# Kernel tuning notes

Measured on AMD Instinct MI355X. Metric: run time of the kernel, lower is better.

Reference implementation:

```python
import jax, jax.numpy as jnp
import numpy as np

NUM_ROUTING = 3
EPS = 1e-9

def squash(s):
    # s: [..., V]; v = s * ||s||^2 / (1+||s||^2) / ||s||
    sq = jnp.sum(s * s, axis=-1, keepdims=True)
    return s * sq / (1.0 + sq) / jnp.sqrt(sq + EPS)

def setup_inputs() -> dict:
    key = jax.random.key(0)
    k1, k2 = jax.random.split(key)
    B, I, U = 128, 2048, 16   # batch, input capsules, input units
    J, V = 32, 16             # output capsules, output units
    x = jax.random.normal(k1, (B, I, U), dtype=jnp.float32)
    W = jax.random.normal(k2, (I, J, V, U), dtype=jnp.float32) * 0.05
    bias = jnp.zeros((J, V), dtype=jnp.float32)
    return {"x": x, "W": W, "bias": bias}

def reference(x, W, bias):
    # Capsule transform: votes u_hat[b,i,j,v] = sum_u x[b,i,u] * W[i,j,v,u]
    u = jnp.einsum('biu,ijvu->bijv', x, W)  # [B, I, J, V]
    b = jnp.zeros(u.shape[:3], dtype=u.dtype)  # routing logits [B, I, J]
    v = None
    for r in range(NUM_ROUTING):
        c = jax.nn.softmax(b, axis=2)                      # coupling over output caps
        s = jnp.einsum('bij,bijv->bjv', c, u) + bias       # [B, J, V]
        v = squash(s)
        if r < NUM_ROUTING - 1:
            b = b + jnp.einsum('bijv,bjv->bij', u, v)      # agreement update
    return v  # activation='linear' -> identity
```

## Files before the change

kernel.cpp:

```cpp
#include <hip/hip_runtime.h>
#include <math.h>

#define NB 128
#define NI 2048
#define NU 16
#define NJ 32
#define NV 16
#define NJV 512

#define BI 16
#define IC (NI / BI)

typedef __attribute__((ext_vector_type(8))) short  short8v;
typedef __attribute__((ext_vector_type(4))) float  float4v;

#define GLD16(gp, lp) __builtin_amdgcn_global_load_lds( \
    (const __attribute__((address_space(1))) unsigned int*)(gp), \
    (__attribute__((address_space(3))) unsigned int*)(lp), 16, 0, 0)

__device__ __forceinline__ unsigned int bf16rne(float f) {
    unsigned int u = __float_as_uint(f);
    return (u + 0x7FFFu + ((u >> 16) & 1u)) >> 16;
}
__device__ __forceinline__ unsigned int bfp(float a, float b) {
    return bf16rne(a) | (bf16rne(b) << 16);
}

__global__ __launch_bounds__(256)
void convert_W_kernel(const float* __restrict__ W, uint4* __restrict__ Wb) {
    int T = blockIdx.x * 256 + threadIdx.x;
    int h = T & 31, t = (T >> 5) & 31, i = T >> 10;
    int c = h & 15, g1 = h >> 4;
    const float* src = W + ((size_t)(i * 512 + t * 16 + c) * 16 + g1 * 8);
    float4 f0 = *(const float4*)src;
    float4 f1 = *(const float4*)(src + 4);
    uint4 o;
    o.x = bfp(f0.x, f0.y); o.y = bfp(f0.z, f0.w);
    o.z = bfp(f1.x, f1.y); o.w = bfp(f1.z, f1.w);
    Wb[T] = o;
}

__global__ __launch_bounds__(256)
void convert_x_kernel(const float* __restrict__ x, uint4* __restrict__ xb) {
    int T = blockIdx.x * 256 + threadIdx.x;
    int h = T & 31, i = (T >> 5) & 2047, bt = T >> 16;
    int c = h & 15, g1 = h >> 4;
    const float* src = x + ((size_t)(bt * 16 + c) * 2048 + i) * 16 + g1 * 8;
    float4 f0 = *(const float4*)src;
    float4 f1 = *(const float4*)(src + 4);
    uint4 o;
    o.x = bfp(f0.x, f0.y); o.y = bfp(f0.z, f0.w);
    o.z = bfp(f1.x, f1.y); o.w = bfp(f1.z, f1.w);
    xb[T] = o;
}

template<int MODE>
__global__ __launch_bounds__(256, 1)
void pass_mfma(const char* __restrict__ Wb, const char* __restrict__ xb,
               const float* __restrict__ Vacc, float* __restrict__ part)
{
    __shared__ float smem[8320];
    const int tid  = threadIdx.x;
    const int lane = tid & 63;
    const int wave = tid >> 6;
    const int c = lane & 15, g = lane >> 4;
    const int jh = wave & 1;
    const int bt = blockIdx.y * 2 + (wave >> 1);
    const int ibase = blockIdx.x * BI;
    const int hh = (g & 1) * 16 + c;

    const char* Bbase = xb + (size_t)bt * 1048576 + (size_t)ibase * 512 + hh * 16;

#define STAGE(i_, buf_)                                                         \
    {                                                                           \
        const char* srcp = Wb + (size_t)(i_) * 16384 + tid * 16;                \
        _Pragma("unroll")                                                       \
        for (int p = 0; p < 4; ++p)                                             \
            GLD16(srcp + p * 4096, &smem[(buf_) * 4096 + p * 1024 + tid * 4]);  \
    }

    STAGE(ibase, 0);
    float4v vc[16];
    if (MODE) {
        const float* vbase = Vacc + ((size_t)(bt * 16 + c) * 512 + jh * 256 + g * 4);
#pragma unroll
        for (int t = 0; t < 16; ++t)
            vc[t] = *reinterpret_cast<const float4v*>(vbase + t * 16);
    }
    short8v bcur = *reinterpret_cast<const short8v*>(Bbase);

    float4v s_loc[16];
#pragma unroll
    for (int t = 0; t < 16; ++t) s_loc[t] = (float4v)(0.f);

    for (int il = 0; il < BI; ++il) {
        const int cur = il & 1;

        if (il < BI - 1) {
            STAGE(ibase + il + 1, cur ^ 1);
            asm volatile("s_waitcnt vmcnt(4)" ::: "memory");
        } else {
            asm volatile("s_waitcnt vmcnt(0)" ::: "memory");
        }
        __builtin_amdgcn_s_barrier();
        asm volatile("" ::: "memory");

        short8v bnxt = bcur;
        if (il < BI - 1)
            bnxt = *reinterpret_cast<const short8v*>(Bbase + (size_t)(il + 1) * 512);

        if (MODE == 0) {
#pragma unroll
            for (int t = 0; t < 16; ++t) {
                short8v a = *reinterpret_cast<const short8v*>(
                    &smem[cur * 4096 + jh * 2048 + t * 128 + hh * 4]);
                s_loc[t] = __builtin_amdgcn_mfma_f32_16x16x32_bf16(a, bcur, s_loc[t], 0, 0, 0);
            }
            asm volatile("s_waitcnt lgkmcnt(0)" ::: "memory");
            __builtin_amdgcn_s_barrier();
            asm volatile("" ::: "memory");
        } else {
            float4v uv[16];
#pragma unroll
            for (int t = 0; t < 16; ++t) {
                short8v a = *reinterpret_cast<const short8v*>(
                    &smem[cur * 4096 + jh * 2048 + t * 128 + hh * 4]);
                uv[t] = __builtin_amdgcn_mfma_f32_16x16x32_bf16(a, bcur, (float4v)(0.f), 0, 0, 0);
            }

            float p[16];
#pragma unroll
            for (int t = 0; t < 16; ++t) {
                float a = uv[t][0] * vc[t][0];
                a = fmaf(uv[t][1], vc[t][1], a);
                a = fmaf(uv[t][2], vc[t][2], a);
                a = fmaf(uv[t][3], vc[t][3], a);
                p[t] = a;
            }
#pragma unroll
            for (int t = 0; t < 16; ++t)
                p[t] += __int_as_float(__builtin_amdgcn_ds_swizzle(__float_as_int(p[t]), 0x401F));
#pragma unroll
            for (int t = 0; t < 16; ++t)
                p[t] += __shfl_xor(p[t], 32, 64);

#pragma unroll
            for (int t = 0; t < 16; ++t) p[t] = __expf(p[t] * 0.5f);
            float s01 = ((p[0] + p[1]) + (p[2] + p[3])) + ((p[4] + p[5]) + (p[6] + p[7]));
            float s23 = ((p[8] + p[9]) + (p[10] + p[11])) + ((p[12] + p[13]) + (p[14] + p[15]));
            float sl = s01 + s23;

            const int par = il & 1;
            if (lane < 16) smem[8192 + par * 64 + wave * 16 + lane] = sl;
            asm volatile("s_waitcnt lgkmcnt(0)" ::: "memory");
            __builtin_amdgcn_s_barrier();
            asm volatile("" ::: "memory");
            float so = smem[8192 + par * 64 + (wave ^ 1) * 16 + c];
            float inv = __builtin_amdgcn_rcpf(sl + so) * 0.5f;

#pragma unroll
            for (int t = 0; t < 16; ++t) {
                float cc = p[t] * inv;
#pragma unroll
                for (int r = 0; r < 4; ++r)
                    s_loc[t][r] = fmaf(cc, uv[t][r], s_loc[t][r]);
            }
        }
        bcur = bnxt;
    }

    const float scale = (MODE == 0) ? (1.0f / 64.0f) : 1.0f;
    float* pb = part + ((size_t)(blockIdx.y * IC + blockIdx.x)) * 16384;
#pragma unroll
    for (int t = 0; t < 16; ++t) {
        float4v o = s_loc[t] * scale;
        *reinterpret_cast<float4v*>(&pb[((wave * 16 + t) * 64 + lane) * 4]) = o;
    }
#undef STAGE
}

__global__ __launch_bounds__(64)
void reduce_squash(const float* __restrict__ part, const float* __restrict__ bias,
                   float* __restrict__ Vacc, float* __restrict__ out, int mode)
{
    const int tid = threadIdx.x;
    const int sfq = blockIdx.x * 64 + tid;
    const int by = sfq >> 12, sf = sfq & 4095;
    const int wave = sf >> 10, t = (sf >> 6) & 15;
    const int c = tid & 15, g = (tid >> 4) & 3;

    const float* src = part + (size_t)by * (IC * 16384) + (size_t)sf * 4;
    float4v a0 = (float4v)(0.f), a1 = (float4v)(0.f), a2 = (float4v)(0.f), a3 = (float4v)(0.f);
    for (int ic = 0; ic < IC; ic += 4) {
        a0 += *reinterpret_cast<const float4v*>(src + (size_t)(ic + 0) * 16384);
        a1 += *reinterpret_cast<const float4v*>(src + (size_t)(ic + 1) * 16384);
        a2 += *reinterpret_cast<const float4v*>(src + (size_t)(ic + 2) * 16384);
        a3 += *reinterpret_cast<const float4v*>(src + (size_t)(ic + 3) * 16384);
    }
    float4v s = (a0 + a1) + (a2 + a3);

    const int b = by * 32 + (wave >> 1) * 16 + c;
    const int j = (wave & 1) * 16 + t;
    const float4v bi = *reinterpret_cast<const float4v*>(bias + j * 16 + g * 4);
    s += bi;

    float sq = s[0]*s[0] + s[1]*s[1] + s[2]*s[2] + s[3]*s[3];
    sq += __int_as_float(__builtin_amdgcn_ds_swizzle(__float_as_int(sq), 0x401F));
    sq += __shfl_xor(sq, 32, 64);

    float m = sq / (1.0f + sq) * __builtin_amdgcn_rsqf(sq + 1e-9f);
    float4v val = s * m;

    float* dst = (mode == 2) ? out : Vacc;
    float4v* dp = reinterpret_cast<float4v*>(dst + (size_t)b * 512 + j * 16 + g * 4);
    if (mode == 1) {
        float4v old = *reinterpret_cast<const float4v*>(
            Vacc + (size_t)b * 512 + j * 16 + g * 4);
        *dp = old + val;
    } else {
        *dp = val;
    }
}

__global__ __launch_bounds__(256)
void squash_kernel(const float* __restrict__ s_in, const float* __restrict__ bias,
                   float* __restrict__ Vacc, float* __restrict__ out, int mode)
{
    int idx = blockIdx.x * 256 + threadIdx.x;
    float s = s_in[idx] + bias[idx & (NJV - 1)];
    float sq = s * s;
#pragma unroll
    for (int m = 1; m < 16; m <<= 1) sq += __shfl_xor(sq, m, 64);
    float val = s * sq / (1.0f + sq) / sqrtf(sq + 1e-9f);
    if (mode == 0)      Vacc[idx] = val;
    else if (mode == 1) Vacc[idx] += val;
    else                out[idx]  = val;
}

#define FBI 16
#define FIC (NI / FBI)

template<int CTRL>
__device__ __forceinline__ float dpp_add(float x) {
    int t = __builtin_amdgcn_update_dpp(0, __float_as_int(x), CTRL, 0xf, 0xf, true);
    return x + __int_as_float(t);
}
__device__ __forceinline__ float red16(float x) {
    x = dpp_add<0xB1>(x); x = dpp_add<0x4E>(x);
    x = dpp_add<0x141>(x); x = dpp_add<0x140>(x);
    return x;
}

template<int MODE>
__global__ __launch_bounds__(256, 1)
void pass_fb(const float* __restrict__ x, const float* __restrict__ W,
             const float* __restrict__ Vacc, float* __restrict__ s_out)
{
    __shared__ float Wlds[2][8192];
    const int tid = threadIdx.x, lane = tid & 63, wave = tid >> 6;
    const int ibase = blockIdx.x * FBI;
    const int b0 = blockIdx.y * 32 + wave * 8;
    const int soff = ((tid >> 4) & 3) * 1024 + (tid & 15) * 64 + (tid >> 6) * 16;
    const char* Wbp = (const char*)W;
#define FSTAGE(i_, buf_) { const char* srcp = Wbp + (size_t)(i_) * 32768 + soff; \
    _Pragma("unroll") for (int p = 0; p < 8; ++p) \
        GLD16(srcp + p * 4096, &Wlds[buf_][p * 1024 + tid * 4]); }
    float vacc[8][8];
    if (MODE) {
#pragma unroll
        for (int b = 0; b < 8; ++b)
#pragma unroll
            for (int k = 0; k < 8; ++k)
                vacc[b][k] = Vacc[(size_t)(b0 + b) * NJV + lane + 64 * k];
    }
    float s_local[8][8];
#pragma unroll
    for (int b = 0; b < 8; ++b)
#pragma unroll
        for (int k = 0; k < 8; ++k) s_local[b][k] = 0.f;
    float uv[8][8];
    FSTAGE(ibase, 0);
    for (int il = 0; il < FBI; ++il) {
        const int i = ibase + il, cur = il & 1;
        if (il < FBI - 1) {
            FSTAGE(i + 1, cur ^ 1);
            asm volatile("s_waitcnt vmcnt(8)" ::: "memory");
        } else {
            asm volatile("s_waitcnt vmcnt(0)" ::: "memory");
        }
        __builtin_amdgcn_s_barrier();
        asm volatile("" ::: "memory");
#pragma unroll
        for (int q = 0; q < 4; ++q) {
            float4 xv[8];
#pragma unroll
            for (int b = 0; b < 8; ++b)
                xv[b] = *(const float4*)(x + ((size_t)(b0 + b) * NI + i) * NU + q * 4);
#pragma unroll
            for (int k = 0; k < 8; ++k) {
                float4 w = *(const float4*)&Wlds[cur][(k * 4 + q) * 256 + lane * 4];
#pragma unroll
                for (int b = 0; b < 8; ++b) {
                    if (MODE) {
                        float a = (q == 0) ? xv[b].x * w.x : fmaf(xv[b].x, w.x, uv[b][k]);
                        a = fmaf(xv[b].y, w.y, a); a = fmaf(xv[b].z, w.z, a);
                        a = fmaf(xv[b].w, w.w, a); uv[b][k] = a;
                    } else {
                        float a = fmaf(xv[b].x, w.x, s_local[b][k]);
                        a = fmaf(xv[b].y, w.y, a); a = fmaf(xv[b].z, w.z, a);
                        a = fmaf(xv[b].w, w.w, a); s_local[b][k] = a;
                    }
                }
            }
        }
        if (MODE) {
#pragma unroll
            for (int b = 0; b < 8; ++b) {
                float p8[8];
#pragma unroll
                for (int k = 0; k < 8; ++k) p8[k] = uv[b][k] * vacc[b][k];
#pragma unroll
                for (int k = 0; k < 8; ++k) p8[k] = red16(p8[k]);
                float sl = 0.f;
#pragma unroll
                for (int k = 0; k < 8; ++k) { p8[k] = __expf(p8[k]); sl += p8[k]; }
                sl += __int_as_float(__builtin_amdgcn_ds_swizzle(__float_as_int(sl), 0x401F));
                sl += __int_as_float(__builtin_amdgcn_ds_bpermute((lane ^ 32) << 2,
                                                                  __float_as_int(sl)));
                float inv = __builtin_amdgcn_rcpf(sl);
#pragma unroll
                for (int k = 0; k < 8; ++k)
                    s_local[b][k] = fmaf(p8[k] * inv, uv[b][k], s_local[b][k]);
            }
        }
        asm volatile("" ::: "memory");
        __builtin_amdgcn_s_barrier();
        asm volatile("" ::: "memory");
    }
    const float scale = (MODE == 0) ? (1.0f / NJ) : 1.0f;
#pragma unroll
    for (int b = 0; b < 8; ++b)
#pragma unroll
        for (int k = 0; k < 8; ++k)
            atomicAdd(&s_out[(size_t)(b0 + b) * NJV + lane + 64 * k],
                      s_local[b][k] * scale);
#undef FSTAGE
}

extern "C" void kernel_launch(void* const* d_in, const int* in_sizes, int n_in,
                              void* d_out, int out_size, void* d_ws, size_t ws_size,
                              hipStream_t stream)
{
    const float* x    = (const float*)d_in[0];
    const float* W    = (const float*)d_in[1];
    const float* bias = (const float*)d_in[2];
    float* out = (float*)d_out;

    float* s_buf = (float*)d_ws;
    float* Vacc  = s_buf + NB * NJV;
    char*  Wb16  = (char*)(Vacc + NB * NJV);
    char*  xb16  = Wb16 + (size_t)33554432;
    float* part  = (float*)(xb16 + (size_t)8388608);

    const size_t NEED = 2u * NB * NJV * 4 + 33554432u + 8388608u + 33554432u;

    dim3 sgrid(NB * NJV / 256), sblk(256);
    size_t s_bytes = (size_t)NB * NJV * sizeof(float);

    if (ws_size >= NEED) {
        convert_W_kernel<<<8192, 256, 0, stream>>>(W, (uint4*)Wb16);
        convert_x_kernel<<<2048, 256, 0, stream>>>(x, (uint4*)xb16);

        dim3 grid(IC, 4), blk(256);
        dim3 rgrid(256), rblk(64);

        pass_mfma<0><<<grid, blk, 0, stream>>>(Wb16, xb16, Vacc, part);
        reduce_squash<<<rgrid, rblk, 0, stream>>>(part, bias, Vacc, out, 0);

        pass_mfma<1><<<grid, blk, 0, stream>>>(Wb16, xb16, Vacc, part);
        reduce_squash<<<rgrid, rblk, 0, stream>>>(part, bias, Vacc, out, 1);

        pass_mfma<1><<<grid, blk, 0, stream>>>(Wb16, xb16, Vacc, part);
        reduce_squash<<<rgrid, rblk, 0, stream>>>(part, bias, Vacc, out, 2);
    } else {
        dim3 grid(FIC, 4), blk(256);

        (void)hipMemsetAsync(s_buf, 0, s_bytes, stream);
        pass_fb<0><<<grid, blk, 0, stream>>>(x, W, Vacc, s_buf);
        squash_kernel<<<sgrid, sblk, 0, stream>>>(s_buf, bias, Vacc, out, 0);

        (void)hipMemsetAsync(s_buf, 0, s_bytes, stream);
        pass_fb<1><<<grid, blk, 0, stream>>>(x, W, Vacc, s_buf);
        squash_kernel<<<sgrid, sblk, 0, stream>>>(s_buf, bias, Vacc, out, 1);

        (void)hipMemsetAsync(s_buf, 0, s_bytes, stream);
        pass_fb<1><<<grid, blk, 0, stream>>>(x, W, Vacc, s_buf);
        squash_kernel<<<sgrid, sblk, 0, stream>>>(s_buf, bias, Vacc, out, 2);
    }
}
```

Measured before the change: 281.8 us.

## Split MFMA pass work across 4 j-quarters per block and parallelize reduction

Each block of the routing pass now handles a single 16-batch tile, with its four waves each covering a quarter of the output capsules, instead of two batch tiles times two j-halves. The grid doubles in y and the launch bounds allow two blocks per CU, cutting per-thread register arrays in half to raise occupancy. The softmax denominator is now combined from four per-wave partial sums in LDS. The reduce kernel uses four waves per block that each sum a quarter of the partial slices and combine them through LDS, giving more parallel loads. In exchange, each W tile staged in LDS is reused by fewer batch tiles, so W is read from L2 twice as often.

```diff
diff --git a/kernel.cpp b/kernel.cpp
--- a/kernel.cpp
+++ b/kernel.cpp
@@ -55,17 +55,16 @@
 }
 
 template<int MODE>
-__global__ __launch_bounds__(256, 1)
+__global__ __launch_bounds__(256, 2)
 void pass_mfma(const char* __restrict__ Wb, const char* __restrict__ xb,
                const float* __restrict__ Vacc, float* __restrict__ part)
 {
     __shared__ float smem[8320];
     const int tid  = threadIdx.x;
     const int lane = tid & 63;
-    const int wave = tid >> 6;
+    const int jq   = tid >> 6;
     const int c = lane & 15, g = lane >> 4;
-    const int jh = wave & 1;
-    const int bt = blockIdx.y * 2 + (wave >> 1);
+    const int bt = blockIdx.y;
     const int ibase = blockIdx.x * BI;
     const int hh = (g & 1) * 16 + c;
 
@@ -80,18 +79,18 @@
     }
 
     STAGE(ibase, 0);
-    float4v vc[16];
+    float4v vc[8];
     if (MODE) {
-        const float* vbase = Vacc + ((size_t)(bt * 16 + c) * 512 + jh * 256 + g * 4);
-#pragma unroll
-        for (int t = 0; t < 16; ++t)
+        const float* vbase = Vacc + ((size_t)(bt * 16 + c) * 512 + jq * 128 + g * 4);
+#pragma unroll
+        for (int t = 0; t < 8; ++t)
             vc[t] = *reinterpret_cast<const float4v*>(vbase + t * 16);
     }
     short8v bcur = *reinterpret_cast<const short8v*>(Bbase);
 
-    float4v s_loc[16];
-#pragma unroll
-    for (int t = 0; t < 16; ++t) s_loc[t] = (float4v)(0.f);
+    float4v s_loc[8];
+#pragma unroll
+    for (int t = 0; t < 8; ++t) s_loc[t] = (float4v)(0.f);
 
     for (int il = 0; il < BI; ++il) {
         const int cur = il & 1;
@@ -111,26 +110,26 @@
 
         if (MODE == 0) {
 #pragma unroll
-            for (int t = 0; t < 16; ++t) {
+            for (int t = 0; t < 8; ++t) {
                 short8v a = *reinterpret_cast<const short8v*>(
-                    &smem[cur * 4096 + jh * 2048 + t * 128 + hh * 4]);
+                    &smem[cur * 4096 + (jq * 8 + t) * 128 + hh * 4]);
                 s_loc[t] = __builtin_amdgcn_mfma_f32_16x16x32_bf16(a, bcur, s_loc[t], 0, 0, 0);
             }
             asm volatile("s_waitcnt lgkmcnt(0)" ::: "memory");
             __builtin_amdgcn_s_barrier();
             asm volatile("" ::: "memory");
         } else {
-            float4v uv[16];
-#pragma unroll
-            for (int t = 0; t < 16; ++t) {
+            float4v uv[8];
+#pragma unroll
+            for (int t = 0; t < 8; ++t) {
                 short8v a = *reinterpret_cast<const short8v*>(
-                    &smem[cur * 4096 + jh * 2048 + t * 128 + hh * 4]);
+                    &smem[cur * 4096 + (jq * 8 + t) * 128 + hh * 4]);
                 uv[t] = __builtin_amdgcn_mfma_f32_16x16x32_bf16(a, bcur, (float4v)(0.f), 0, 0, 0);
             }
 
-            float p[16];
-#pragma unroll
-            for (int t = 0; t < 16; ++t) {
+            float p[8];
+#pragma unroll
+            for (int t = 0; t < 8; ++t) {
                 float a = uv[t][0] * vc[t][0];
                 a = fmaf(uv[t][1], vc[t][1], a);
                 a = fmaf(uv[t][2], vc[t][2], a);
@@ -138,28 +137,29 @@
                 p[t] = a;
             }
 #pragma unroll
-            for (int t = 0; t < 16; ++t)
+            for (int t = 0; t < 8; ++t)
                 p[t] += __int_as_float(__builtin_amdgcn_ds_swizzle(__float_as_int(p[t]), 0x401F));
 #pragma unroll
-            for (int t = 0; t < 16; ++t)
+            for (int t = 0; t < 8; ++t)
                 p[t] += __shfl_xor(p[t], 32, 64);
 
 #pragma unroll
-            for (int t = 0; t < 16; ++t) p[t] = __expf(p[t] * 0.5f);
-            float s01 = ((p[0] + p[1]) + (p[2] + p[3])) + ((p[4] + p[5]) + (p[6] + p[7]));
-            float s23 = ((p[8] + p[9]) + (p[10] + p[11])) + ((p[12] + p[13]) + (p[14] + p[15]));
-            float sl = s01 + s23;
+            for (int t = 0; t < 8; ++t) p[t] = __expf(p[t] * 0.5f);
+            float sl = ((p[0] + p[1]) + (p[2] + p[3])) + ((p[4] + p[5]) + (p[6] + p[7]));
 
             const int par = il & 1;
-            if (lane < 16) smem[8192 + par * 64 + wave * 16 + lane] = sl;
+            if (lane < 16) smem[8192 + par * 64 + jq * 16 + lane] = sl;
             asm volatile("s_waitcnt lgkmcnt(0)" ::: "memory");
             __builtin_amdgcn_s_barrier();
             asm volatile("" ::: "memory");
-            float so = smem[8192 + par * 64 + (wave ^ 1) * 16 + c];
-            float inv = __builtin_amdgcn_rcpf(sl + so) * 0.5f;
-
-#pragma unroll
-            for (int t = 0; t < 16; ++t) {
+            float q0 = smem[8192 + par * 64 + 0 * 16 + c];
+            float q1 = smem[8192 + par * 64 + 1 * 16 + c];
+            float q2 = smem[8192 + par * 64 + 2 * 16 + c];
+            float q3 = smem[8192 + par * 64 + 3 * 16 + c];
+            float inv = __builtin_amdgcn_rcpf((q0 + q1) + (q2 + q3)) * 0.5f;
+
+#pragma unroll
+            for (int t = 0; t < 8; ++t) {
                 float cc = p[t] * inv;
 #pragma unroll
                 for (int r = 0; r < 4; ++r)
@@ -170,55 +170,71 @@
     }
 
     const float scale = (MODE == 0) ? (1.0f / 64.0f) : 1.0f;
-    float* pb = part + ((size_t)(blockIdx.y * IC + blockIdx.x)) * 16384;
-#pragma unroll
-    for (int t = 0; t < 16; ++t) {
+    float* pb = part + ((size_t)(blockIdx.y * IC + blockIdx.x)) * 8192;
+#pragma unroll
+    for (int t = 0; t < 8; ++t) {
         float4v o = s_loc[t] * scale;
-        *reinterpret_cast<float4v*>(&pb[((wave * 16 + t) * 64 + lane) * 4]) = o;
+        *reinterpret_cast<float4v*>(&pb[((jq * 8 + t) * 64 + lane) * 4]) = o;
     }
 #undef STAGE
 }
 
-__global__ __launch_bounds__(64)
+__global__ __launch_bounds__(256)
 void reduce_squash(const float* __restrict__ part, const float* __restrict__ bias,
                    float* __restrict__ Vacc, float* __restrict__ out, int mode)
 {
+    __shared__ float lds[3][64][4];
     const int tid = threadIdx.x;
-    const int sfq = blockIdx.x * 64 + tid;
-    const int by = sfq >> 12, sf = sfq & 4095;
-    const int wave = sf >> 10, t = (sf >> 6) & 15;
-    const int c = tid & 15, g = (tid >> 4) & 3;
-
-    const float* src = part + (size_t)by * (IC * 16384) + (size_t)sf * 4;
-    float4v a0 = (float4v)(0.f), a1 = (float4v)(0.f), a2 = (float4v)(0.f), a3 = (float4v)(0.f);
-    for (int ic = 0; ic < IC; ic += 4) {
-        a0 += *reinterpret_cast<const float4v*>(src + (size_t)(ic + 0) * 16384);
-        a1 += *reinterpret_cast<const float4v*>(src + (size_t)(ic + 1) * 16384);
-        a2 += *reinterpret_cast<const float4v*>(src + (size_t)(ic + 2) * 16384);
-        a3 += *reinterpret_cast<const float4v*>(src + (size_t)(ic + 3) * 16384);
+    const int w = tid >> 6, l = tid & 63;
+    const int sfq = blockIdx.x * 64 + l;
+    const int bt = sfq >> 11, sf = sfq & 2047;
+    const int j = sf >> 6;
+    const int c = l & 15, g = (l >> 4) & 3;
+
+    const float* src = part + (size_t)bt * (IC * 8192) + (size_t)sf * 4
+                            + (size_t)(w * 32) * 8192;
+    float4v a0 = (float4v)(0.f), a1 = (float4v)(0.f),
+            a2 = (float4v)(0.f), a3 = (float4v)(0.f);
+#pragma unroll
+    for (int ic = 0; ic < 32; ic += 4) {
+        a0 += *reinterpret_cast<const float4v*>(src + (size_t)(ic + 0) * 8192);
+        a1 += *reinterpret_cast<const float4v*>(src + (size_t)(ic + 1) * 8192);
+        a2 += *reinterpret_cast<const float4v*>(src + (size_t)(ic + 2) * 8192);
+        a3 += *reinterpret_cast<const float4v*>(src + (size_t)(ic + 3) * 8192);
     }
     float4v s = (a0 + a1) + (a2 + a3);
 
-    const int b = by * 32 + (wave >> 1) * 16 + c;
-    const int j = (wave & 1) * 16 + t;
-    const float4v bi = *reinterpret_cast<const float4v*>(bias + j * 16 + g * 4);
-    s += bi;
-
-    float sq = s[0]*s[0] + s[1]*s[1] + s[2]*s[2] + s[3]*s[3];
-    sq += __int_as_float(__builtin_amdgcn_ds_swizzle(__float_as_int(sq), 0x401F));
-    sq += __shfl_xor(sq, 32, 64);
-
-    float m = sq / (1.0f + sq) * __builtin_amdgcn_rsqf(sq + 1e-9f);
-    float4v val = s * m;
-
-    float* dst = (mode == 2) ? out : Vacc;
-    float4v* dp = reinterpret_cast<float4v*>(dst + (size_t)b * 512 + j * 16 + g * 4);
-    if (mode == 1) {
-        float4v old = *reinterpret_cast<const float4v*>(
-            Vacc + (size_t)b * 512 + j * 16 + g * 4);
-        *dp = old + val;
-    } else {
-        *dp = val;
+    if (w != 0) {
+        lds[w - 1][l][0] = s[0]; lds[w - 1][l][1] = s[1];
+        lds[w - 1][l][2] = s[2]; lds[w - 1][l][3] = s[3];
+    }
+    __syncthreads();
+    if (w == 0) {
+#pragma unroll
+        for (int q = 0; q < 3; ++q) {
+            s[0] += lds[q][l][0]; s[1] += lds[q][l][1];
+            s[2] += lds[q][l][2]; s[3] += lds[q][l][3];
+        }
+        const float4v bi = *reinterpret_cast<const float4v*>(bias + j * 16 + g * 4);
+        s += bi;
+
+        float sq = s[0]*s[0] + s[1]*s[1] + s[2]*s[2] + s[3]*s[3];
+        sq += __int_as_float(__builtin_amdgcn_ds_swizzle(__float_as_int(sq), 0x401F));
+        sq += __shfl_xor(sq, 32, 64);
+
+        float m = sq / (1.0f + sq) * __builtin_amdgcn_rsqf(sq + 1e-9f);
+        float4v val = s * m;
+
+        const int b = bt * 16 + c;
+        float* dst = (mode == 2) ? out : Vacc;
+        float4v* dp = reinterpret_cast<float4v*>(dst + (size_t)b * 512 + j * 16 + g * 4);
+        if (mode == 1) {
+            float4v old = *reinterpret_cast<const float4v*>(
+                Vacc + (size_t)b * 512 + j * 16 + g * 4);
+            *dp = old + val;
+        } else {
+            *dp = val;
+        }
     }
 }
 
@@ -371,8 +387,8 @@
         convert_W_kernel<<<8192, 256, 0, stream>>>(W, (uint4*)Wb16);
         convert_x_kernel<<<2048, 256, 0, stream>>>(x, (uint4*)xb16);
 
-        dim3 grid(IC, 4), blk(256);
-        dim3 rgrid(256), rblk(64);
+        dim3 grid(IC, 8), blk(256);
+        dim3 rgrid(256), rblk(256);
 
         pass_mfma<0><<<grid, blk, 0, stream>>>(Wb16, xb16, Vacc, part);
         reduce_squash<<<rgrid, rblk, 0, stream>>>(part, bias, Vacc, out, 0);
```

Result: faster. 237.3 us (-15.8%).
